# Kernel tuning notes

Hardware: AMD Instinct MI355X
Metric: run time of the kernel (lower is better)

## Reference

```python
import jax, jax.numpy as jnp
import numpy as np


def _proj(x_flat, w, b):
    # x_flat: (N, C, L), w: (O, C), b: (O,) -> (N, O, L)  (1x1x1 Conv3d)
    return jnp.einsum('oc,ncl->nol', w, x_flat) + b[None, :, None]


def setup_inputs() -> dict:
    key = jax.random.key(0)
    ks = jax.random.split(key, 9)
    C, Ch = 256, 128
    N, T, H, W = 2, 8, 28, 28
    s_in = 1.0 / np.sqrt(C)
    s_h = 1.0 / np.sqrt(Ch)
    return {
        'x': jax.random.normal(ks[0], (N, C, T, H, W), jnp.float32),
        'g_w': jax.random.normal(ks[1], (Ch, C), jnp.float32) * s_in,
        'g_b': jax.random.normal(ks[2], (Ch,), jnp.float32) * 0.01,
        'theta_w': jax.random.normal(ks[3], (Ch, C), jnp.float32) * s_in,
        'theta_b': jax.random.normal(ks[4], (Ch,), jnp.float32) * 0.01,
        'phi_w': jax.random.normal(ks[5], (Ch, C), jnp.float32) * s_in,
        'phi_b': jax.random.normal(ks[6], (Ch,), jnp.float32) * 0.01,
        'wz_w': jax.random.normal(ks[7], (C, Ch), jnp.float32) * s_h,
        'wz_b': jax.random.normal(ks[8], (C,), jnp.float32) * 0.01,
    }


def reference(x, g_w, g_b, theta_w, theta_b, phi_w, phi_b, wz_w, wz_b):
    N, C, T, H, W = x.shape
    L = T * H * W
    xf = x.reshape(N, C, L)                      # (N, C, L)
    g_x = _proj(xf, g_w, g_b)                    # (N, Ch, L)
    theta_x = _proj(xf, theta_w, theta_b)        # (N, Ch, L)
    phi_x = _proj(xf, phi_w, phi_b)              # (N, Ch, L)
    # f[n, i, j] = theta[n, :, i] . phi[n, :, j]
    f = jnp.einsum('nci,ncj->nij', theta_x, phi_x)  # (N, L, L)
    f = jax.nn.softmax(f, axis=-1)
    # y[n, c, i] = sum_j f[n, i, j] * g[n, c, j]
    y = jnp.einsum('nij,ncj->nci', f, g_x)          # (N, Ch, L)
    z = _proj(y, wz_w, wz_b)                        # (N, C, L)
    return z.reshape(N, C, T, H, W) + x
```

## Files before the change

kernel.cpp:

```cpp
#include <hip/hip_runtime.h>
#include <hip/hip_bf16.h>

constexpr int CIN    = 256;
constexpr int CH     = 128;
constexpr int LSEQ   = 6272;
constexpr int NBATCH = 2;
constexpr int NLCH   = NBATCH * LSEQ * CH;
constexpr float SHIFT = 40.0f;

typedef __attribute__((ext_vector_type(8))) __bf16 bf16x8;
typedef __attribute__((ext_vector_type(4))) float  f32x4;

__device__ __forceinline__ float bf_lo(unsigned u) { return __uint_as_float(u << 16); }
__device__ __forceinline__ float bf_hi(unsigned u) { return __uint_as_float(u & 0xffff0000u); }
__device__ __forceinline__ unsigned short f2bf(float f) {
    __hip_bfloat16 h = __float2bfloat16(f);
    return *reinterpret_cast<unsigned short*>(&h);
}
__device__ __forceinline__ float us2f(unsigned short h) {
    return __uint_as_float((unsigned)h << 16);
}

union BF8 { bf16x8 v; unsigned short u[8]; };

__device__ __forceinline__ void split8(float4 a, float4 b, bf16x8& hi, bf16x8& lo) {
    BF8 H, L;
    float f[8] = { a.x, a.y, a.z, a.w, b.x, b.y, b.z, b.w };
    #pragma unroll
    for (int p = 0; p < 8; ++p) {
        unsigned short h = f2bf(f[p]);
        H.u[p] = h;
        L.u[p] = f2bf(f[p] - us2f(h));
    }
    hi = H.v; lo = L.v;
}

#define GLDS16(g, l) __builtin_amdgcn_global_load_lds(                      \
    (const __attribute__((address_space(1))) void*)(g),                     \
    (__attribute__((address_space(3))) void*)(l), 16, 0, 0)

__global__ __launch_bounds__(256) void proj_kernel(
    const float* __restrict__ x,
    const float* __restrict__ th_w, const float* __restrict__ th_b,
    const float* __restrict__ ph_w, const float* __restrict__ ph_b,
    const float* __restrict__ gw,   const float* __restrict__ gb,
    unsigned short* __restrict__ q, unsigned short* __restrict__ k,
    unsigned short* __restrict__ vt)
{
    constexpr int XS = 264;
    __shared__ unsigned short xhi[64][XS];
    __shared__ unsigned short xlo[64][XS];
    unsigned short (*gst)[137] = (unsigned short (*)[137])&xhi[0][0];

    const int t    = threadIdx.x;
    const int n    = blockIdx.y;
    const int l0   = blockIdx.x * 64;
    const int w    = t >> 6;
    const int lane = t & 63;
    const int lo   = lane & 15;
    const int quad = lane >> 4;

    {
        const int c = t;
        const float4* xr = (const float4*)(x + (size_t)(n * CIN + c) * LSEQ + l0);
        #pragma unroll
        for (int g4 = 0; g4 < 16; ++g4) {
            float4 v = xr[g4];
            float f[4] = { v.x, v.y, v.z, v.w };
            #pragma unroll
            for (int j = 0; j < 4; ++j) {
                unsigned short h = f2bf(f[j]);
                xhi[g4 * 4 + j][c] = h;
                xlo[g4 * 4 + j][c] = f2bf(f[j] - us2f(h));
            }
        }
    }

    const float* wrp[6]; float biasv[6];
    #pragma unroll
    for (int j = 0; j < 6; ++j) {
        int gch = 96 * w + 16 * j + lo;
        if (gch < 128)      { wrp[j] = th_w + (size_t)gch * CIN;         biasv[j] = th_b[gch]; }
        else if (gch < 256) { wrp[j] = ph_w + (size_t)(gch - 128) * CIN; biasv[j] = ph_b[gch - 128]; }
        else                { wrp[j] = gw   + (size_t)(gch - 256) * CIN; biasv[j] = gb[gch - 256]; }
    }

    f32x4 acc[4][6];
    #pragma unroll
    for (int mt = 0; mt < 4; ++mt)
        #pragma unroll
        for (int j = 0; j < 6; ++j) acc[mt][j] = (f32x4){0.f, 0.f, 0.f, 0.f};

    __syncthreads();

    for (int ks = 0; ks < 8; ++ks) {
        const int k0 = ks * 32 + quad * 8;
        bf16x8 ahi[4], alo[4];
        #pragma unroll
        for (int mt = 0; mt < 4; ++mt) {
            ahi[mt] = *(const bf16x8*)&xhi[mt * 16 + lo][k0];
            alo[mt] = *(const bf16x8*)&xlo[mt * 16 + lo][k0];
        }
        #pragma unroll
        for (int j = 0; j < 6; ++j) {
            const float* p = wrp[j] + k0;
            bf16x8 bhi, blo;
            split8(*(const float4*)p, *(const float4*)(p + 4), bhi, blo);
            #pragma unroll
            for (int mt = 0; mt < 4; ++mt) {
                f32x4 a = acc[mt][j];
                a = __builtin_amdgcn_mfma_f32_16x16x32_bf16(ahi[mt], bhi, a, 0, 0, 0);
                a = __builtin_amdgcn_mfma_f32_16x16x32_bf16(alo[mt], bhi, a, 0, 0, 0);
                a = __builtin_amdgcn_mfma_f32_16x16x32_bf16(ahi[mt], blo, a, 0, 0, 0);
                acc[mt][j] = a;
            }
        }
    }

    __syncthreads();

    #pragma unroll
    for (int j = 0; j < 6; ++j) {
        const int base = 96 * w + 16 * j;
        #pragma unroll
        for (int mt = 0; mt < 4; ++mt) {
            #pragma unroll
            for (int r = 0; r < 4; ++r) {
                float val = acc[mt][j][r] + biasv[j];
                const int lrow = mt * 16 + quad * 4 + r;
                if (base < 256) {
                    unsigned short* dst = (base < 128) ? q : k;
                    const int ch = (base < 128) ? base + lo : base - 128 + lo;
                    dst[(size_t)(n * LSEQ + l0 + lrow) * CH + ch] = f2bf(val);
                } else {
                    gst[lrow][base - 256 + lo] = f2bf(val);
                }
            }
        }
    }
    __syncthreads();

    #pragma unroll
    for (int rep = 0; rep < 16; ++rep) {
        const int flat = rep * 256 + t;
        const int ch   = flat >> 5;
        const int lam  = flat & 31;
        unsigned u = (unsigned)gst[2 * lam][ch] | ((unsigned)gst[2 * lam + 1][ch] << 16);
        ((unsigned*)(vt + (size_t)(n * CH + ch) * LSEQ + l0))[lam] = u;
    }
}

__global__ __launch_bounds__(256, 2) void attn_kernel(
    const unsigned short* __restrict__ qb, const unsigned short* __restrict__ kb,
    const unsigned short* __restrict__ vtg,
    float* __restrict__ Op, float* __restrict__ lp,
    unsigned short* __restrict__ yb, int ns)
{
    constexpr int NTJ = LSEQ / 64;
    __shared__ unsigned short ks [2][64][128];
    __shared__ unsigned short vTs[2][128][64];
    __shared__ unsigned short ps [4][32][64];

    const int t    = threadIdx.x;
    const int s    = blockIdx.y;
    const int n    = blockIdx.z;
    const int i0   = blockIdx.x * 128;
    const int w    = t >> 6;
    const int lane = t & 63;
    const int lo   = lane & 15;
    const int quad = lane >> 4;
    const int lom  = (lo & 7) * 4;

    const int jt0 = (s * NTJ) / ns;
    const int jt1 = ((s + 1) * NTJ) / ns;

    const unsigned short* kbase = kb  + (size_t)n * LSEQ * CH;
    const unsigned short* vbase = vtg + (size_t)n * CH * LSEQ;

    bf16x8 qfrag[2][4];
    #pragma unroll
    for (int mt = 0; mt < 2; ++mt) {
        const unsigned short* qrow =
            qb + (size_t)(n * LSEQ + i0 + 32 * w + mt * 16 + lo) * CH;
        #pragma unroll
        for (int kc = 0; kc < 4; ++kc)
            qfrag[mt][kc] = *(const bf16x8*)(qrow + kc * 32 + quad * 8);
    }

    f32x4 o_acc[2][8];
    #pragma unroll
    for (int mt = 0; mt < 2; ++mt)
        #pragma unroll
        for (int nt = 0; nt < 8; ++nt) o_acc[mt][nt] = (f32x4){0.f, 0.f, 0.f, 0.f};
    float l_r[2][4] = {{0.f,0.f,0.f,0.f},{0.f,0.f,0.f,0.f}};

    auto stage = [&](int buf, int jt) {
        const int j0 = jt * 64;
        #pragma unroll
        for (int i = 0; i < 4; ++i) {
            const int c = w * 4 + i;
            {
                const int row = c * 4 + (lane >> 4);
                const int pcol = (lane & 15) * 4;
                const int lcol = pcol ^ ((row & 7) * 4);
                const unsigned short* g = kbase + (size_t)(j0 + row) * CH + lcol * 2;
                GLDS16(g, &ks[buf][0][0] + c * 512);
            }
            {
                const int row = c * 8 + (lane >> 3);
                const int pcol = (lane & 7) * 4;
                const int lcol = pcol ^ ((row & 7) * 4);
                const unsigned short* g = vbase + (size_t)row * LSEQ + j0 + lcol * 2;
                GLDS16(g, &vTs[buf][0][0] + c * 512);
            }
        }
    };

    int buf = 0;
    stage(0, jt0);
    __syncthreads();

    for (int jt = jt0; jt < jt1; ++jt) {
        if (jt + 1 < jt1) stage(buf ^ 1, jt + 1);

        f32x4 sacc[2][4];
        #pragma unroll
        for (int mt = 0; mt < 2; ++mt)
            #pragma unroll
            for (int ct = 0; ct < 4; ++ct) sacc[mt][ct] = (f32x4){0.f,0.f,0.f,0.f};
        #pragma unroll
        for (int ct = 0; ct < 4; ++ct) {
            #pragma unroll
            for (int kc = 0; kc < 4; ++kc) {
                const int pcol = (kc * 16 + quad * 4) ^ lom;
                bf16x8 b = *(const bf16x8*)&ks[buf][ct * 16 + lo][pcol * 2];
                #pragma unroll
                for (int mt = 0; mt < 2; ++mt)
                    sacc[mt][ct] = __builtin_amdgcn_mfma_f32_16x16x32_bf16(
                        qfrag[mt][kc], b, sacc[mt][ct], 0, 0, 0);
            }
        }

        __builtin_amdgcn_wave_barrier();
        #pragma unroll
        for (int mt = 0; mt < 2; ++mt) {
            #pragma unroll
            for (int ct = 0; ct < 4; ++ct) {
                #pragma unroll
                for (int r = 0; r < 4; ++r) {
                    float p = __expf(sacc[mt][ct][r] - SHIFT);
                    l_r[mt][r] += p;
                    const int row = mt * 16 + quad * 4 + r;
                    const int pdw = (ct * 8 + (lo >> 1)) ^ ((row & 7) * 4);
                    ps[w][row][pdw * 2 + (lo & 1)] = f2bf(p);
                }
            }
        }
        __builtin_amdgcn_wave_barrier();
        __builtin_amdgcn_s_waitcnt(0xC07F);

        bf16x8 pfrag[2][2];
        #pragma unroll
        for (int mt = 0; mt < 2; ++mt)
            #pragma unroll
            for (int kc = 0; kc < 2; ++kc) {
                const int pcol = (kc * 16 + quad * 4) ^ lom;
                pfrag[mt][kc] = *(const bf16x8*)&ps[w][mt * 16 + lo][pcol * 2];
            }

        #pragma unroll
        for (int nt = 0; nt < 8; ++nt) {
            #pragma unroll
            for (int kc = 0; kc < 2; ++kc) {
                const int pcol = (kc * 16 + quad * 4) ^ lom;
                bf16x8 b = *(const bf16x8*)&vTs[buf][nt * 16 + lo][pcol * 2];
                #pragma unroll
                for (int mt = 0; mt < 2; ++mt)
                    o_acc[mt][nt] = __builtin_amdgcn_mfma_f32_16x16x32_bf16(
                        pfrag[mt][kc], b, o_acc[mt][nt], 0, 0, 0);
            }
        }

        __syncthreads();
        buf ^= 1;
    }

    #pragma unroll
    for (int mt = 0; mt < 2; ++mt)
        #pragma unroll
        for (int r = 0; r < 4; ++r) {
            #pragma unroll
            for (int off = 1; off < 16; off <<= 1)
                l_r[mt][r] += __shfl_xor(l_r[mt][r], off);
        }

    if (Op != nullptr) {
        #pragma unroll
        for (int mt = 0; mt < 2; ++mt)
            #pragma unroll
            for (int r = 0; r < 4; ++r) {
                const int qi = i0 + 32 * w + mt * 16 + quad * 4 + r;
                float* orow = Op + ((size_t)(n * ns + s) * LSEQ + qi) * CH;
                #pragma unroll
                for (int nt = 0; nt < 8; ++nt)
                    orow[nt * 16 + lo] = o_acc[mt][nt][r];
                if (lo == 0)
                    lp[(size_t)(n * ns + s) * LSEQ + qi] = l_r[mt][r];
            }
    } else {
        #pragma unroll
        for (int mt = 0; mt < 2; ++mt)
            #pragma unroll
            for (int r = 0; r < 4; ++r) {
                const int qi = i0 + 32 * w + mt * 16 + quad * 4 + r;
                const float inv = 1.0f / l_r[mt][r];
                unsigned short* yr = yb + (size_t)(n * LSEQ + qi) * CH;
                #pragma unroll
                for (int nt = 0; nt < 8; ++nt)
                    yr[nt * 16 + lo] = f2bf(o_acc[mt][nt][r] * inv);
            }
    }
}

__global__ __launch_bounds__(256) void combine_kernel(
    const float* __restrict__ Op, const float* __restrict__ lp,
    unsigned short* __restrict__ yb, int ns)
{
    const int idx = blockIdx.x * 256 + threadIdx.x;
    const int n   = idx / (LSEQ * 32);
    const int rem = idx - n * (LSEQ * 32);
    const int l   = rem >> 5;
    const int c4  = (rem & 31) << 2;

    float4 o = make_float4(0.f, 0.f, 0.f, 0.f);
    float ls = 0.f;
    for (int s = 0; s < ns; ++s) {
        const float4 v = *(const float4*)&Op[((size_t)(n * ns + s) * LSEQ + l) * CH + c4];
        o.x += v.x; o.y += v.y; o.z += v.z; o.w += v.w;
        ls += lp[(size_t)(n * ns + s) * LSEQ + l];
    }
    const float inv = 1.0f / ls;
    unsigned r0 = (unsigned)f2bf(o.x * inv) | ((unsigned)f2bf(o.y * inv) << 16);
    unsigned r1 = (unsigned)f2bf(o.z * inv) | ((unsigned)f2bf(o.w * inv) << 16);
    uint2* dst = (uint2*)(yb + (size_t)(n * LSEQ + l) * CH + c4);
    *dst = make_uint2(r0, r1);
}

__global__ __launch_bounds__(256) void zout_kernel(
    const unsigned short* __restrict__ yb,
    const float* __restrict__ wz_w, const float* __restrict__ wz_b,
    const float* __restrict__ x, float* __restrict__ out)
{
    const int t    = threadIdx.x;
    const int n    = blockIdx.y;
    const int l0   = blockIdx.x * 64;
    const int w    = t >> 6;
    const int lane = t & 63;
    const int lo   = lane & 15;
    const int quad = lane >> 4;

    f32x4 acc[4][4];
    #pragma unroll
    for (int mt = 0; mt < 4; ++mt)
        #pragma unroll
        for (int nt = 0; nt < 4; ++nt) acc[mt][nt] = (f32x4){0.f, 0.f, 0.f, 0.f};

    const unsigned short* yrow[4];
    #pragma unroll
    for (int nt = 0; nt < 4; ++nt)
        yrow[nt] = yb + (size_t)(n * LSEQ + l0 + nt * 16 + lo) * CH;

    #pragma unroll
    for (int ks = 0; ks < 4; ++ks) {
        const int k0 = ks * 32 + quad * 8;
        bf16x8 bfr[4];
        #pragma unroll
        for (int nt = 0; nt < 4; ++nt)
            bfr[nt] = *(const bf16x8*)(yrow[nt] + k0);
        #pragma unroll
        for (int mt = 0; mt < 4; ++mt) {
            const float* p = wz_w + (size_t)(64 * w + mt * 16 + lo) * CH + k0;
            bf16x8 ahi, alo;
            split8(*(const float4*)p, *(const float4*)(p + 4), ahi, alo);
            #pragma unroll
            for (int nt = 0; nt < 4; ++nt) {
                f32x4 a = acc[mt][nt];
                a = __builtin_amdgcn_mfma_f32_16x16x32_bf16(ahi, bfr[nt], a, 0, 0, 0);
                a = __builtin_amdgcn_mfma_f32_16x16x32_bf16(alo, bfr[nt], a, 0, 0, 0);
                acc[mt][nt] = a;
            }
        }
    }

    #pragma unroll
    for (int mt = 0; mt < 4; ++mt) {
        #pragma unroll
        for (int r = 0; r < 4; ++r) {
            const int c = 64 * w + mt * 16 + quad * 4 + r;
            const float bias = wz_b[c];
            const size_t base = (size_t)(n * CIN + c) * LSEQ + l0;
            #pragma unroll
            for (int nt = 0; nt < 4; ++nt) {
                const size_t off = base + nt * 16 + lo;
                out[off] = acc[mt][nt][r] + bias + x[off];
            }
        }
    }
}

extern "C" void kernel_launch(void* const* d_in, const int* in_sizes, int n_in,
                              void* d_out, int out_size, void* d_ws, size_t ws_size,
                              hipStream_t stream) {
    const float* x    = (const float*)d_in[0];
    const float* g_w  = (const float*)d_in[1];
    const float* g_b  = (const float*)d_in[2];
    const float* th_w = (const float*)d_in[3];
    const float* th_b = (const float*)d_in[4];
    const float* ph_w = (const float*)d_in[5];
    const float* ph_b = (const float*)d_in[6];
    const float* wz_w = (const float*)d_in[7];
    const float* wz_b = (const float*)d_in[8];
    float* out = (float*)d_out;

    unsigned short* q  = (unsigned short*)d_ws;
    unsigned short* k  = q + NLCH;
    unsigned short* vt = k + NLCH;
    unsigned short* y  = vt + NLCH;

    const size_t base = (size_t)4 * NLCH * 2;
    const size_t per  = (size_t)NLCH * 4 + (size_t)NBATCH * LSEQ * 4;
    int ns = 0;
    if      (ws_size >= base + 4 * per) ns = 4;
    else if (ws_size >= base + 2 * per) ns = 2;
    else if (ws_size >= base + 1 * per) ns = 1;

    float* Op = (ns > 0) ? (float*)(y + NLCH) : nullptr;
    float* lp = (ns > 0) ? Op + (size_t)ns * NLCH : nullptr;

    proj_kernel<<<dim3(LSEQ / 64, NBATCH), 256, 0, stream>>>(
        x, th_w, th_b, ph_w, ph_b, g_w, g_b, q, k, vt);

    if (ns > 0) {
        attn_kernel<<<dim3(LSEQ / 128, ns, NBATCH), 256, 0, stream>>>(
            q, k, vt, Op, lp, y, ns);
        combine_kernel<<<(NBATCH * LSEQ * 32) / 256, 256, 0, stream>>>(Op, lp, y, ns);
    } else {
        attn_kernel<<<dim3(LSEQ / 128, 1, NBATCH), 256, 0, stream>>>(
            q, k, vt, nullptr, nullptr, y, 1);
    }

    zout_kernel<<<dim3(LSEQ / 64, NBATCH), 256, 0, stream>>>(y, wz_w, wz_b, x, out);
}
```

Measured before the change: 190.9 us.

## Compute transposed S=K·Qᵀ, build P in registers, single-buffer LDS, raise occupancy

The QK product is now computed as K times Q transposed, so the softmax probabilities sit in registers in a layout that can be packed with v_cvt_pk_bf16_f32 and rearranged with permlane swaps straight into MFMA A-fragments. This drops the per-wave P round trip through shared memory. K and V staging becomes single-buffered, with the next K and V tiles loaded right after each barrier, and launch bounds go from 2 to 4 blocks per CU. The split count can now reach 8 when workspace allows, raising combine traffic. The cost is less overlap of loads with compute and added register pressure at the higher occupancy.

```diff
diff --git a/kernel.cpp b/kernel.cpp
--- a/kernel.cpp
+++ b/kernel.cpp
@@ -22,6 +22,19 @@
 }
 
 union BF8 { bf16x8 v; unsigned short u[8]; };
+union PU  { unsigned u[4]; bf16x8 v; };
+
+__device__ __forceinline__ unsigned cvtpk(float a, float b) {
+    unsigned r;
+    asm("v_cvt_pk_bf16_f32 %0, %1, %2" : "=v"(r) : "v"(a), "v"(b));
+    return r;
+}
+__device__ __forceinline__ void pl32swap(unsigned &a, unsigned &b) {
+    asm("v_permlane32_swap_b32 %0, %1" : "+v"(a), "+v"(b));
+}
+__device__ __forceinline__ void pl16swap(unsigned &a, unsigned &b) {
+    asm("v_permlane16_swap_b32 %0, %1" : "+v"(a), "+v"(b));
+}
 
 __device__ __forceinline__ void split8(float4 a, float4 b, bf16x8& hi, bf16x8& lo) {
     BF8 H, L;
@@ -150,16 +163,15 @@
     }
 }
 
-__global__ __launch_bounds__(256, 2) void attn_kernel(
+__global__ __launch_bounds__(256, 4) void attn_kernel(
     const unsigned short* __restrict__ qb, const unsigned short* __restrict__ kb,
     const unsigned short* __restrict__ vtg,
     float* __restrict__ Op, float* __restrict__ lp,
     unsigned short* __restrict__ yb, int ns)
 {
     constexpr int NTJ = LSEQ / 64;
-    __shared__ unsigned short ks [2][64][128];
-    __shared__ unsigned short vTs[2][128][64];
-    __shared__ unsigned short ps [4][32][64];
+    __shared__ unsigned short ksm[64][128];
+    __shared__ unsigned short vsm[128][64];
 
     const int t    = threadIdx.x;
     const int s    = blockIdx.y;
@@ -179,12 +191,12 @@
 
     bf16x8 qfrag[2][4];
     #pragma unroll
-    for (int mt = 0; mt < 2; ++mt) {
+    for (int nt = 0; nt < 2; ++nt) {
         const unsigned short* qrow =
-            qb + (size_t)(n * LSEQ + i0 + 32 * w + mt * 16 + lo) * CH;
+            qb + (size_t)(n * LSEQ + i0 + 32 * w + nt * 16 + lo) * CH;
         #pragma unroll
         for (int kc = 0; kc < 4; ++kc)
-            qfrag[mt][kc] = *(const bf16x8*)(qrow + kc * 32 + quad * 8);
+            qfrag[nt][kc] = *(const bf16x8*)(qrow + kc * 32 + quad * 8);
     }
 
     f32x4 o_acc[2][8];
@@ -192,88 +204,88 @@
     for (int mt = 0; mt < 2; ++mt)
         #pragma unroll
         for (int nt = 0; nt < 8; ++nt) o_acc[mt][nt] = (f32x4){0.f, 0.f, 0.f, 0.f};
-    float l_r[2][4] = {{0.f,0.f,0.f,0.f},{0.f,0.f,0.f,0.f}};
-
-    auto stage = [&](int buf, int jt) {
+    float l_r[2] = {0.f, 0.f};
+
+    auto stageK = [&](int jt) {
         const int j0 = jt * 64;
         #pragma unroll
         for (int i = 0; i < 4; ++i) {
             const int c = w * 4 + i;
-            {
-                const int row = c * 4 + (lane >> 4);
-                const int pcol = (lane & 15) * 4;
-                const int lcol = pcol ^ ((row & 7) * 4);
-                const unsigned short* g = kbase + (size_t)(j0 + row) * CH + lcol * 2;
-                GLDS16(g, &ks[buf][0][0] + c * 512);
-            }
-            {
-                const int row = c * 8 + (lane >> 3);
-                const int pcol = (lane & 7) * 4;
-                const int lcol = pcol ^ ((row & 7) * 4);
-                const unsigned short* g = vbase + (size_t)row * LSEQ + j0 + lcol * 2;
-                GLDS16(g, &vTs[buf][0][0] + c * 512);
-            }
+            const int row = c * 4 + (lane >> 4);
+            const int pcol = (lane & 15) * 4;
+            const int lcol = pcol ^ ((row & 7) * 4);
+            GLDS16(kbase + (size_t)(j0 + row) * CH + lcol * 2, &ksm[0][0] + c * 512);
         }
     };
-
-    int buf = 0;
-    stage(0, jt0);
+    auto stageV = [&](int jt) {
+        const int j0 = jt * 64;
+        #pragma unroll
+        for (int i = 0; i < 4; ++i) {
+            const int c = w * 4 + i;
+            const int row = c * 8 + (lane >> 3);
+            const int pcol = (lane & 7) * 4;
+            const int lcol = pcol ^ ((row & 7) * 4);
+            GLDS16(vbase + (size_t)row * LSEQ + j0 + lcol * 2, &vsm[0][0] + c * 512);
+        }
+    };
+
+    stageK(jt0);
+    stageV(jt0);
     __syncthreads();
 
     for (int jt = jt0; jt < jt1; ++jt) {
-        if (jt + 1 < jt1) stage(buf ^ 1, jt + 1);
-
-        f32x4 sacc[2][4];
-        #pragma unroll
-        for (int mt = 0; mt < 2; ++mt)
-            #pragma unroll
-            for (int ct = 0; ct < 4; ++ct) sacc[mt][ct] = (f32x4){0.f,0.f,0.f,0.f};
-        #pragma unroll
-        for (int ct = 0; ct < 4; ++ct) {
-            #pragma unroll
-            for (int kc = 0; kc < 4; ++kc) {
-                const int pcol = (kc * 16 + quad * 4) ^ lom;
-                bf16x8 b = *(const bf16x8*)&ks[buf][ct * 16 + lo][pcol * 2];
+        f32x4 sacc[4][2];
+        #pragma unroll
+        for (int mt = 0; mt < 4; ++mt)
+            #pragma unroll
+            for (int nt = 0; nt < 2; ++nt) sacc[mt][nt] = (f32x4){0.f,0.f,0.f,0.f};
+        #pragma unroll
+        for (int kc = 0; kc < 4; ++kc) {
+            const int pcol = (kc * 16 + quad * 4) ^ lom;
+            #pragma unroll
+            for (int mt = 0; mt < 4; ++mt) {
+                bf16x8 a = *(const bf16x8*)&ksm[mt * 16 + lo][pcol * 2];
                 #pragma unroll
-                for (int mt = 0; mt < 2; ++mt)
-                    sacc[mt][ct] = __builtin_amdgcn_mfma_f32_16x16x32_bf16(
-                        qfrag[mt][kc], b, sacc[mt][ct], 0, 0, 0);
-            }
-        }
-
-        __builtin_amdgcn_wave_barrier();
-        #pragma unroll
-        for (int mt = 0; mt < 2; ++mt) {
-            #pragma unroll
-            for (int ct = 0; ct < 4; ++ct) {
+                for (int nt = 0; nt < 2; ++nt)
+                    sacc[mt][nt] = __builtin_amdgcn_mfma_f32_16x16x32_bf16(
+                        a, qfrag[nt][kc], sacc[mt][nt], 0, 0, 0);
+            }
+        }
+
+        bf16x8 pfrag[2][2];
+        #pragma unroll
+        for (int nt = 0; nt < 2; ++nt) {
+            #pragma unroll
+            for (int kc = 0; kc < 2; ++kc) {
+                float e[8];
                 #pragma unroll
-                for (int r = 0; r < 4; ++r) {
-                    float p = __expf(sacc[mt][ct][r] - SHIFT);
-                    l_r[mt][r] += p;
-                    const int row = mt * 16 + quad * 4 + r;
-                    const int pdw = (ct * 8 + (lo >> 1)) ^ ((row & 7) * 4);
-                    ps[w][row][pdw * 2 + (lo & 1)] = f2bf(p);
-                }
-            }
-        }
-        __builtin_amdgcn_wave_barrier();
-        __builtin_amdgcn_s_waitcnt(0xC07F);
-
-        bf16x8 pfrag[2][2];
-        #pragma unroll
-        for (int mt = 0; mt < 2; ++mt)
+                for (int h = 0; h < 2; ++h)
+                    #pragma unroll
+                    for (int r = 0; r < 4; ++r) {
+                        float p = __expf(sacc[2 * kc + h][nt][r] - SHIFT);
+                        l_r[nt] += p;
+                        e[h * 4 + r] = p;
+                    }
+                unsigned A0 = cvtpk(e[0], e[1]);
+                unsigned A1 = cvtpk(e[2], e[3]);
+                unsigned B0 = cvtpk(e[4], e[5]);
+                unsigned B1 = cvtpk(e[6], e[7]);
+                pl32swap(A0, B0); pl16swap(A0, B0);
+                pl32swap(A1, B1); pl16swap(A1, B1);
+                PU pu; pu.u[0] = A0; pu.u[1] = A1; pu.u[2] = B0; pu.u[3] = B1;
+                pfrag[nt][kc] = pu.v;
+            }
+        }
+
+        __syncthreads();
+        if (jt + 1 < jt1) stageK(jt + 1);
+
+        #pragma unroll
+        for (int nt = 0; nt < 8; ++nt) {
             #pragma unroll
             for (int kc = 0; kc < 2; ++kc) {
                 const int pcol = (kc * 16 + quad * 4) ^ lom;
-                pfrag[mt][kc] = *(const bf16x8*)&ps[w][mt * 16 + lo][pcol * 2];
-            }
-
-        #pragma unroll
-        for (int nt = 0; nt < 8; ++nt) {
-            #pragma unroll
-            for (int kc = 0; kc < 2; ++kc) {
-                const int pcol = (kc * 16 + quad * 4) ^ lom;
-                bf16x8 b = *(const bf16x8*)&vTs[buf][nt * 16 + lo][pcol * 2];
+                bf16x8 b = *(const bf16x8*)&vsm[nt * 16 + lo][pcol * 2];
                 #pragma unroll
                 for (int mt = 0; mt < 2; ++mt)
                     o_acc[mt][nt] = __builtin_amdgcn_mfma_f32_16x16x32_bf16(
@@ -282,17 +294,14 @@
         }
 
         __syncthreads();
-        buf ^= 1;
-    }
-
-    #pragma unroll
-    for (int mt = 0; mt < 2; ++mt)
-        #pragma unroll
-        for (int r = 0; r < 4; ++r) {
-            #pragma unroll
-            for (int off = 1; off < 16; off <<= 1)
-                l_r[mt][r] += __shfl_xor(l_r[mt][r], off);
-        }
+        if (jt + 1 < jt1) stageV(jt + 1);
+    }
+
+    #pragma unroll
+    for (int nt = 0; nt < 2; ++nt) {
+        l_r[nt] += __shfl_xor(l_r[nt], 16);
+        l_r[nt] += __shfl_xor(l_r[nt], 32);
+    }
 
     if (Op != nullptr) {
         #pragma unroll
@@ -300,12 +309,13 @@
             #pragma unroll
             for (int r = 0; r < 4; ++r) {
                 const int qi = i0 + 32 * w + mt * 16 + quad * 4 + r;
+                const float lsum = __shfl(l_r[mt], quad * 4 + r);
                 float* orow = Op + ((size_t)(n * ns + s) * LSEQ + qi) * CH;
                 #pragma unroll
                 for (int nt = 0; nt < 8; ++nt)
                     orow[nt * 16 + lo] = o_acc[mt][nt][r];
                 if (lo == 0)
-                    lp[(size_t)(n * ns + s) * LSEQ + qi] = l_r[mt][r];
+                    lp[(size_t)(n * ns + s) * LSEQ + qi] = lsum;
             }
     } else {
         #pragma unroll
@@ -313,7 +323,8 @@
             #pragma unroll
             for (int r = 0; r < 4; ++r) {
                 const int qi = i0 + 32 * w + mt * 16 + quad * 4 + r;
-                const float inv = 1.0f / l_r[mt][r];
+                const float lsum = __shfl(l_r[mt], quad * 4 + r);
+                const float inv = 1.0f / lsum;
                 unsigned short* yr = yb + (size_t)(n * LSEQ + qi) * CH;
                 #pragma unroll
                 for (int nt = 0; nt < 8; ++nt)
@@ -430,9 +441,10 @@
     const size_t base = (size_t)4 * NLCH * 2;
     const size_t per  = (size_t)NLCH * 4 + (size_t)NBATCH * LSEQ * 4;
     int ns = 0;
-    if      (ws_size >= base + 4 * per) ns = 4;
-    else if (ws_size >= base + 2 * per) ns = 2;
-    else if (ws_size >= base + 1 * per) ns = 1;
+    if (ws_size > base) {
+        size_t cap = (ws_size - base) / per;
+        ns = (cap > 8) ? 8 : (int)cap;
+    }
 
     float* Op = (ns > 0) ? (float*)(y + NLCH) : nullptr;
     float* lp = (ns > 0) ? Op + (size_t)ns * NLCH : nullptr;
```

New measurement: 293.5 us. +53.8%, slower.
